# Performance work log

Hardware: AMD Instinct MI355X
Metric: run time of the kernel (lower is better)

Reference implementation:

```python
import jax, jax.numpy as jnp
import numpy as np

FILTER_K = 100  # filter_K from __init__
NUM_CLASSES = 1000


def setup_inputs() -> dict:
    key = jax.random.key(0)
    ks = jax.random.split(key, 7)
    B, Din, D, C, N = 256, 2048, 512, NUM_CLASSES, 50000
    x = jax.random.normal(ks[0], (B, Din), jnp.float32)
    Wf = jax.random.normal(ks[1], (Din, D), jnp.float32) * 0.02
    Wc = jax.random.normal(ks[2], (C, D), jnp.float32) * 0.05
    bc = jax.random.normal(ks[3], (C,), jnp.float32) * 0.01
    supports_in = jax.random.normal(ks[4], (N, D), jnp.float32)
    ent_in = jax.random.uniform(ks[5], (N,), jnp.float32)
    labels_idx = jax.random.randint(ks[6], (N,), 0, C)
    return {"x": x, "Wf": Wf, "Wc": Wc, "bc": bc,
            "supports_in": supports_in, "ent_in": ent_in, "labels_idx": labels_idx}


def _softmax_entropy(logits):
    # -(softmax * log_softmax).sum(1), computed stably in one pass
    logp = jax.nn.log_softmax(logits, axis=1)
    return -(jnp.exp(logp) * logp).sum(axis=1)


def reference(x, Wf, Wc, bc, supports_in, ent_in, labels_idx):
    C = Wc.shape[0]
    z = x @ Wf                    # featurizer: [B, D]
    p = z @ Wc.T + bc             # classifier logits: [B, C]
    yhat = jax.nn.one_hot(jnp.argmax(p, axis=1), C, dtype=z.dtype)
    ent_new = _softmax_entropy(p)
    labels_in = jax.nn.one_hot(labels_idx, C, dtype=z.dtype)

    # grow support memory
    supports = jnp.concatenate([supports_in, z], axis=0)   # [M, D]
    labels = jnp.concatenate([labels_in, yhat], axis=0)    # [M, C]
    ent = jnp.concatenate([ent_in, ent_new], axis=0)       # [M]

    # select_supports: per-class keep FILTER_K lowest-entropy entries.
    # Torch gathers a variable-size subset; equivalent fixed-shape form is a
    # boolean mask (non-selected rows contribute zero to the weights matmul).
    y = jnp.argmax(labels, axis=1)
    M = ent.shape[0]
    order = jnp.lexsort((ent, y))            # sort by class, then entropy
    y_sorted = y[order]
    # rank of each entry within its class segment
    rank = jnp.arange(M) - jnp.searchsorted(y_sorted, y_sorted, side='left')
    mask = jnp.zeros((M,), bool).at[order].set(rank < FILTER_K)
    maskf = mask.astype(z.dtype)

    # normalize supports row-wise (F.normalize, eps=1e-12), then masked matmul
    s_norm = supports / jnp.maximum(
        jnp.linalg.norm(supports, axis=1, keepdims=True), 1e-12)
    weights = (s_norm * maskf[:, None]).T @ (labels * maskf[:, None])  # [D, C]
    weights = weights / jnp.maximum(
        jnp.linalg.norm(weights, axis=0, keepdims=True), 1e-12)
    return z @ weights            # [B, C]
```

## Files before the change

kernel.cpp:

```cpp
#include <hip/hip_runtime.h>
#include <hip/hip_bf16.h>
#include <math.h>

#define BB   256
#define DIN  2048
#define DD   512
#define CC   1000
#define NN   50000
#define MM   (NN + BB)
#define FILTER_K 100
#define SLOT 512

#define SK1  32
#define SKP  8

#define Z_OFF     0
#define CNT_OFF   (Z_OFF + BB*DD)
#define ENTS_OFF  (CNT_OFF + 1024)
#define IDXS_OFF  (ENTS_OFF + CC*SLOT)
#define WN_OFF    (IDXS_OFF + CC*SLOT)
#define ZP_OFF    (WN_OFF + CC*DD)
#define PP_OFF    (ZP_OFF + SK1*BB*DD)

__global__ __launch_bounds__(256, 2) void fused_scatter_gemm_ab(
    const float* __restrict__ A, const float* __restrict__ B,
    float* __restrict__ Cp,
    const int* __restrict__ labels_idx, const float* __restrict__ ent_in,
    int* __restrict__ cnt, float* __restrict__ ent_s,
    int* __restrict__ idx_s) {
  __shared__ float As[16][68];
  __shared__ float Bs[16][132];
  const int gbid = blockIdx.x, tid = threadIdx.x;
  if (gbid >= 512) {
    int m = (gbid - 512) * 256 + tid;
    if (m < NN) {
      int c = labels_idx[m];
      int pos = atomicAdd(&cnt[c], 1);
      if (pos < SLOT) {
        ent_s[(size_t)c * SLOT + pos] = ent_in[m];
        idx_s[(size_t)c * SLOT + pos] = m;
      }
    }
    return;
  }
  const int m0 = ((gbid >> 2) & 3) * 64;
  const int n0 = (gbid & 3) * 128;
  const int k0 = (gbid >> 4) * 64;
  const int ar = tid >> 2, ac = (tid & 3) * 4;
  const int br = tid >> 4, bcn = (tid & 15) * 8;
  const int tm = (tid >> 4) * 4, tn = (tid & 15) * 4;
  float acc[4][8] = {};
  float4 av  = *(const float4*)&A[(size_t)(m0 + ar) * DIN + k0 + ac];
  float4 bv0 = *(const float4*)&B[(size_t)(k0 + br) * DD + n0 + bcn];
  float4 bv1 = *(const float4*)&B[(size_t)(k0 + br) * DD + n0 + bcn + 4];
  for (int kk = 0; kk < 64; kk += 16) {
    __syncthreads();
    As[ac + 0][ar] = av.x; As[ac + 1][ar] = av.y;
    As[ac + 2][ar] = av.z; As[ac + 3][ar] = av.w;
    *(float4*)&Bs[br][bcn] = bv0;
    *(float4*)&Bs[br][bcn + 4] = bv1;
    __syncthreads();
    if (kk + 16 < 64) {
      av  = *(const float4*)&A[(size_t)(m0 + ar) * DIN + k0 + kk + 16 + ac];
      bv0 = *(const float4*)&B[(size_t)(k0 + kk + 16 + br) * DD + n0 + bcn];
      bv1 = *(const float4*)&B[(size_t)(k0 + kk + 16 + br) * DD + n0 + bcn + 4];
    }
#pragma unroll
    for (int q = 0; q < 16; ++q) {
      float4 a  = *(const float4*)&As[q][tm];
      float4 b0 = *(const float4*)&Bs[q][tn];
      float4 b1 = *(const float4*)&Bs[q][tn + 64];
      float aa[4] = {a.x, a.y, a.z, a.w};
      float bb[8] = {b0.x, b0.y, b0.z, b0.w, b1.x, b1.y, b1.z, b1.w};
#pragma unroll
      for (int i = 0; i < 4; ++i)
#pragma unroll
        for (int j = 0; j < 8; ++j) acc[i][j] += aa[i] * bb[j];
    }
  }
  float* Cb = Cp + (size_t)(gbid >> 4) * BB * DD;
#pragma unroll
  for (int i = 0; i < 4; ++i) {
    *(float4*)&Cb[(size_t)(m0 + tm + i) * DD + n0 + tn] =
        make_float4(acc[i][0], acc[i][1], acc[i][2], acc[i][3]);
    *(float4*)&Cb[(size_t)(m0 + tm + i) * DD + n0 + 64 + tn] =
        make_float4(acc[i][4], acc[i][5], acc[i][6], acc[i][7]);
  }
}

template <int S>
__global__ __launch_bounds__(256) void reduce_part(
    const float* __restrict__ part, float* __restrict__ out, int n4) {
  int i = blockIdx.x * 256 + threadIdx.x;
  if (i >= n4) return;
  const float4* p4 = (const float4*)part;
  float4 a = p4[i];
#pragma unroll
  for (int s = 1; s < S; ++s) {
    float4 b = p4[(size_t)s * n4 + i];
    a.x += b.x; a.y += b.y; a.z += b.z; a.w += b.w;
  }
  ((float4*)out)[i] = a;
}

__global__ __launch_bounds__(256, 2) void gemm_abt_part(
    const float* __restrict__ A, const float* __restrict__ Bm,
    float* __restrict__ Cp) {
  __shared__ float As[16][68];
  __shared__ float Bs[16][68];
  const int tid = threadIdx.x;
  const int m0 = blockIdx.y * 64;
  const int n0 = blockIdx.x * 64;
  const int k0 = blockIdx.z * 64;
  const int ar = tid >> 2, ac = (tid & 3) * 4;
  const int tm = (tid >> 4) * 4, tn = (tid & 15) * 4;
  float acc[4][4] = {};
  float4 av = *(const float4*)&A[(size_t)(m0 + ar) * DD + k0 + ac];
  float4 bv = make_float4(0.f, 0.f, 0.f, 0.f);
  if (n0 + ar < CC) bv = *(const float4*)&Bm[(size_t)(n0 + ar) * DD + k0 + ac];
  for (int kk = 0; kk < 64; kk += 16) {
    __syncthreads();
    As[ac + 0][ar] = av.x; As[ac + 1][ar] = av.y;
    As[ac + 2][ar] = av.z; As[ac + 3][ar] = av.w;
    Bs[ac + 0][ar] = bv.x; Bs[ac + 1][ar] = bv.y;
    Bs[ac + 2][ar] = bv.z; Bs[ac + 3][ar] = bv.w;
    __syncthreads();
    if (kk + 16 < 64) {
      av = *(const float4*)&A[(size_t)(m0 + ar) * DD + k0 + kk + 16 + ac];
      if (n0 + ar < CC)
        bv = *(const float4*)&Bm[(size_t)(n0 + ar) * DD + k0 + kk + 16 + ac];
    }
#pragma unroll
    for (int q = 0; q < 16; ++q) {
      float4 a = *(const float4*)&As[q][tm];
      float4 b = *(const float4*)&Bs[q][tn];
      float aa[4] = {a.x, a.y, a.z, a.w};
      float bb[4] = {b.x, b.y, b.z, b.w};
#pragma unroll
      for (int i = 0; i < 4; ++i)
#pragma unroll
        for (int j = 0; j < 4; ++j) acc[i][j] += aa[i] * bb[j];
    }
  }
  float* Cb = Cp + (size_t)blockIdx.z * BB * CC;
#pragma unroll
  for (int i = 0; i < 4; ++i) {
    int n = n0 + tn;
    if (n + 3 < CC) {
      *(float4*)&Cb[(size_t)(m0 + tm + i) * CC + n] =
          make_float4(acc[i][0], acc[i][1], acc[i][2], acc[i][3]);
    } else {
#pragma unroll
      for (int j = 0; j < 4; ++j)
        if (n + j < CC) Cb[(size_t)(m0 + tm + i) * CC + n + j] = acc[i][j];
    }
  }
}

__global__ __launch_bounds__(256) void rowstats(
    const float* __restrict__ ppart, const float* __restrict__ bc,
    int* __restrict__ cnt, float* __restrict__ ent_s,
    int* __restrict__ idx_s) {
  const int b = blockIdx.x, tid = threadIdx.x;
  const int lane = tid & 63, wid = tid >> 6;
  float r[4];
  float mv = -INFINITY; int mi = 0x7fffffff;
#pragma unroll
  for (int i = 0; i < 4; ++i) {
    int c = tid + 256 * i;
    if (c < CC) {
      float v = bc[c];
#pragma unroll
      for (int s = 0; s < SKP; ++s)
        v += ppart[(size_t)s * BB * CC + (size_t)b * CC + c];
      r[i] = v;
    } else r[i] = -INFINITY;
    if (r[i] > mv) { mv = r[i]; mi = c; }
  }
#pragma unroll
  for (int o = 32; o > 0; o >>= 1) {
    float ov = __shfl_down(mv, o, 64);
    int oi = __shfl_down(mi, o, 64);
    if (ov > mv || (ov == mv && oi < mi)) { mv = ov; mi = oi; }
  }
  __shared__ float smv[4]; __shared__ int smi[4];
  __shared__ float ssm[4], tsm[4];
  if (lane == 0) { smv[wid] = mv; smi[wid] = mi; }
  __syncthreads();
  if (tid == 0) {
#pragma unroll
    for (int w = 1; w < 4; ++w)
      if (smv[w] > smv[0] || (smv[w] == smv[0] && smi[w] < smi[0])) {
        smv[0] = smv[w]; smi[0] = smi[w];
      }
  }
  __syncthreads();
  const float m = smv[0]; const int am = smi[0];
  float s = 0.f, t = 0.f;
#pragma unroll
  for (int i = 0; i < 4; ++i) {
    if (tid + 256 * i < CC) {
      float u = r[i] - m;
      float e = expf(u);
      s += e; t += u * e;
    }
  }
#pragma unroll
  for (int o = 32; o > 0; o >>= 1) {
    s += __shfl_down(s, o, 64);
    t += __shfl_down(t, o, 64);
  }
  if (lane == 0) { ssm[wid] = s; tsm[wid] = t; }
  __syncthreads();
  if (tid == 0) {
    float S = ssm[0] + ssm[1] + ssm[2] + ssm[3];
    float T = tsm[0] + tsm[1] + tsm[2] + tsm[3];
    float ent = logf(S) - T / S;
    int pos = atomicAdd(&cnt[am], 1);
    if (pos < SLOT) {
      ent_s[(size_t)am * SLOT + pos] = ent;
      idx_s[(size_t)am * SLOT + pos] = NN + b;
    }
  }
}

__global__ __launch_bounds__(256) void class_weights(
    const float* __restrict__ supports_in, const float* __restrict__ z,
    const float* __restrict__ ent_s, const int* __restrict__ idx_s,
    const int* __restrict__ cnt, float* __restrict__ wn) {
  const int c = blockIdx.x, tid = threadIdx.x;
  const int lane = tid & 63, wid = tid >> 6;
  int n = cnt[c]; if (n > SLOT) n = SLOT;

  __shared__ int sel[SLOT];
  __shared__ float se[SLOT];
  __shared__ int si[SLOT];
  int seln;
  if (n <= FILTER_K) {
    seln = n;
    for (int i = tid; i < n; i += 256) sel[i] = idx_s[(size_t)c * SLOT + i];
  } else {
    for (int i = tid; i < SLOT; i += 256) {
      if (i < n) { se[i] = ent_s[(size_t)c * SLOT + i]; si[i] = idx_s[(size_t)c * SLOT + i]; }
      else       { se[i] = INFINITY;                     si[i] = 0x7fffffff; }
    }
    __syncthreads();
    for (int k = 2; k <= SLOT; k <<= 1)
      for (int j = k >> 1; j > 0; j >>= 1) {
        for (int i = tid; i < SLOT; i += 256) {
          int ixj = i ^ j;
          if (ixj > i) {
            bool up = ((i & k) == 0);
            float e1 = se[i], e2 = se[ixj];
            int i1 = si[i], i2 = si[ixj];
            bool gt = (e1 > e2) || (e1 == e2 && i1 > i2);
            if (gt == up) { se[i] = e2; se[ixj] = e1; si[i] = i2; si[ixj] = i1; }
          }
        }
        __syncthreads();
      }
    seln = FILTER_K;
    for (int i = tid; i < FILTER_K; i += 256) sel[i] = si[i];
  }
  __syncthreads();
  const int seln_pad = (seln + 15) & ~15;
  if (seln > 0)
    for (int i = seln + tid; i < seln_pad; i += 256) sel[i] = sel[0];
  __syncthreads();

  float4 a0 = make_float4(0.f, 0.f, 0.f, 0.f), a1 = a0;
  for (int t = wid * 4; t < seln_pad; t += 16) {
    float4 u0[4], u1[4]; float s[4];
#pragma unroll
    for (int j = 0; j < 4; ++j) {
      int r = sel[t + j];
      const float4* p4 = (const float4*)((r < NN)
          ? supports_in + (size_t)r * DD : z + (size_t)(r - NN) * DD);
      u0[j] = p4[lane * 2]; u1[j] = p4[lane * 2 + 1];
    }
#pragma unroll
    for (int j = 0; j < 4; ++j)
      s[j] = u0[j].x * u0[j].x + u0[j].y * u0[j].y + u0[j].z * u0[j].z
           + u0[j].w * u0[j].w + u1[j].x * u1[j].x + u1[j].y * u1[j].y
           + u1[j].z * u1[j].z + u1[j].w * u1[j].w;
#pragma unroll
    for (int o = 1; o < 64; o <<= 1) {
#pragma unroll
      for (int j = 0; j < 4; ++j) s[j] += __shfl_xor(s[j], o, 64);
    }
#pragma unroll
    for (int j = 0; j < 4; ++j) {
      float sc = (t + j < seln) ? 1.0f / fmaxf(sqrtf(s[j]), 1e-12f) : 0.f;
      a0.x += u0[j].x * sc; a0.y += u0[j].y * sc;
      a0.z += u0[j].z * sc; a0.w += u0[j].w * sc;
      a1.x += u1[j].x * sc; a1.y += u1[j].y * sc;
      a1.z += u1[j].z * sc; a1.w += u1[j].w * sc;
    }
  }

  __shared__ float part[4][DD];
  *(float4*)&part[wid][lane * 8] = a0;
  *(float4*)&part[wid][lane * 8 + 4] = a1;
  __syncthreads();
  const int d = tid * 2;
  float wx = part[0][d] + part[1][d] + part[2][d] + part[3][d];
  float wy = part[0][d + 1] + part[1][d + 1] + part[2][d + 1] + part[3][d + 1];
  float ss = wx * wx + wy * wy;
#pragma unroll
  for (int o = 1; o < 64; o <<= 1) ss += __shfl_xor(ss, o, 64);
  __shared__ float tot[4];
  if (lane == 0) tot[wid] = ss;
  __syncthreads();
  float S = tot[0] + tot[1] + tot[2] + tot[3];
  float sc = 1.0f / fmaxf(sqrtf(S), 1e-12f);
  ((float2*)(wn + (size_t)c * DD))[tid] = make_float2(wx * sc, wy * sc);
}

__global__ __launch_bounds__(256, 2) void gemm_out(
    const float* __restrict__ A, const float* __restrict__ Bm,
    float* __restrict__ C) {
  __shared__ float As[16][36];
  __shared__ float Bs[16][68];
  const int tid = threadIdx.x;
  const int m0 = blockIdx.y * 32;
  const int n0 = blockIdx.x * 64;
  const int ar = tid >> 3, ac = (tid & 7) * 2;
  const int br = tid >> 2, bc = (tid & 3) * 4;
  const int tm = (tid >> 4) * 2, tn = (tid & 15) * 4;
  float acc[2][4] = {};
  float2 av = *(const float2*)&A[(size_t)(m0 + ar) * DD + ac];
  float4 bv = make_float4(0.f, 0.f, 0.f, 0.f);
  if (n0 + br < CC) bv = *(const float4*)&Bm[(size_t)(n0 + br) * DD + bc];
  for (int k0 = 0; k0 < DD; k0 += 16) {
    __syncthreads();
    As[ac + 0][ar] = av.x; As[ac + 1][ar] = av.y;
    Bs[bc + 0][br] = bv.x; Bs[bc + 1][br] = bv.y;
    Bs[bc + 2][br] = bv.z; Bs[bc + 3][br] = bv.w;
    __syncthreads();
    if (k0 + 16 < DD) {
      av = *(const float2*)&A[(size_t)(m0 + ar) * DD + k0 + 16 + ac];
      if (n0 + br < CC)
        bv = *(const float4*)&Bm[(size_t)(n0 + br) * DD + k0 + 16 + bc];
    }
#pragma unroll
    for (int q = 0; q < 16; ++q) {
      float2 a = *(const float2*)&As[q][tm];
      float4 b = *(const float4*)&Bs[q][tn];
      float aa[2] = {a.x, a.y};
      float bb[4] = {b.x, b.y, b.z, b.w};
#pragma unroll
      for (int i = 0; i < 2; ++i)
#pragma unroll
        for (int j = 0; j < 4; ++j) acc[i][j] += aa[i] * bb[j];
    }
  }
#pragma unroll
  for (int i = 0; i < 2; ++i) {
    int n = n0 + tn;
    if (n + 3 < CC) {
      *(float4*)&C[(size_t)(m0 + tm + i) * CC + n] =
          make_float4(acc[i][0], acc[i][1], acc[i][2], acc[i][3]);
    } else {
#pragma unroll
      for (int j = 0; j < 4; ++j)
        if (n + j < CC) C[(size_t)(m0 + tm + i) * CC + n + j] = acc[i][j];
    }
  }
}

extern "C" void kernel_launch(void* const* d_in, const int* in_sizes, int n_in,
                              void* d_out, int out_size, void* d_ws, size_t ws_size,
                              hipStream_t stream) {
  (void)in_sizes; (void)n_in; (void)out_size; (void)ws_size;
  const float* x           = (const float*)d_in[0];
  const float* Wf          = (const float*)d_in[1];
  const float* Wc          = (const float*)d_in[2];
  const float* bc          = (const float*)d_in[3];
  const float* supports_in = (const float*)d_in[4];
  const float* ent_in      = (const float*)d_in[5];
  const int*   labels_idx  = (const int*)d_in[6];
  float* out = (float*)d_out;

  float* W = (float*)d_ws;
  float* z     = W + Z_OFF;
  int*   cnt   = (int*)(W + CNT_OFF);
  float* ent_s = W + ENTS_OFF;
  int*   idx_s = (int*)(W + IDXS_OFF);
  float* wn    = W + WN_OFF;
  float* zpart = W + ZP_OFF;
  float* ppart = W + PP_OFF;

  hipMemsetAsync(cnt, 0, 1024 * sizeof(int), stream);
  fused_scatter_gemm_ab<<<512 + (NN + 255) / 256, 256, 0, stream>>>(
      x, Wf, zpart, labels_idx, ent_in, cnt, ent_s, idx_s);
  reduce_part<SK1><<<(BB * DD / 4 + 255) / 256, 256, 0, stream>>>(
      zpart, z, BB * DD / 4);
  gemm_abt_part<<<dim3((CC + 63) / 64, BB / 64, SKP), 256, 0, stream>>>(
      z, Wc, ppart);
  rowstats<<<BB, 256, 0, stream>>>(ppart, bc, cnt, ent_s, idx_s);
  class_weights<<<CC, 256, 0, stream>>>(supports_in, z, ent_s, idx_s, cnt, wn);
  gemm_out<<<dim3((CC + 63) / 64, BB / 32), 256, 0, stream>>>(z, wn, out);
}
```

Baseline: 228.3 us.

## Halve split-K partitions, pad atomic counters, pack entropy-index pairs as float2

Doubles the per-block K extent in both split-K GEMMs, halving the number of partial buffers and the reduction work in reduce_part and rowstats. Spreads per-class atomic counters across 16-int strides so that atomics on different classes do not contend on the same cache line. Stores each entropy/index pair as one float2 so that scatter and gather use one 8-byte access instead of two separate arrays. The cost is fewer blocks per GEMM, and therefore less parallelism, plus a larger counter memset.

```diff
diff --git a/kernel.cpp b/kernel.cpp
--- a/kernel.cpp
+++ b/kernel.cpp
@@ -10,15 +10,15 @@
 #define MM   (NN + BB)
 #define FILTER_K 100
 #define SLOT 512
-
-#define SK1  32
-#define SKP  8
+#define CSTRIDE 16
+
+#define SK1  16
+#define SKP  4
 
 #define Z_OFF     0
 #define CNT_OFF   (Z_OFF + BB*DD)
-#define ENTS_OFF  (CNT_OFF + 1024)
-#define IDXS_OFF  (ENTS_OFF + CC*SLOT)
-#define WN_OFF    (IDXS_OFF + CC*SLOT)
+#define EI_OFF    (CNT_OFF + 1024*CSTRIDE)
+#define WN_OFF    (EI_OFF + CC*SLOT*2)
 #define ZP_OFF    (WN_OFF + CC*DD)
 #define PP_OFF    (ZP_OFF + SK1*BB*DD)
 
@@ -26,26 +26,25 @@
     const float* __restrict__ A, const float* __restrict__ B,
     float* __restrict__ Cp,
     const int* __restrict__ labels_idx, const float* __restrict__ ent_in,
-    int* __restrict__ cnt, float* __restrict__ ent_s,
-    int* __restrict__ idx_s) {
+    int* __restrict__ cnt, float2* __restrict__ ei) {
   __shared__ float As[16][68];
   __shared__ float Bs[16][132];
   const int gbid = blockIdx.x, tid = threadIdx.x;
-  if (gbid >= 512) {
-    int m = (gbid - 512) * 256 + tid;
+  if (gbid >= 256) {
+    int m = (gbid - 256) * 256 + tid;
     if (m < NN) {
       int c = labels_idx[m];
-      int pos = atomicAdd(&cnt[c], 1);
+      int pos = atomicAdd(&cnt[c * CSTRIDE], 1);
       if (pos < SLOT) {
-        ent_s[(size_t)c * SLOT + pos] = ent_in[m];
-        idx_s[(size_t)c * SLOT + pos] = m;
+        float2 pr; pr.x = ent_in[m]; pr.y = __int_as_float(m);
+        ei[(size_t)c * SLOT + pos] = pr;
       }
     }
     return;
   }
   const int m0 = ((gbid >> 2) & 3) * 64;
   const int n0 = (gbid & 3) * 128;
-  const int k0 = (gbid >> 4) * 64;
+  const int k0 = (gbid >> 4) * 128;
   const int ar = tid >> 2, ac = (tid & 3) * 4;
   const int br = tid >> 4, bcn = (tid & 15) * 8;
   const int tm = (tid >> 4) * 4, tn = (tid & 15) * 4;
@@ -53,14 +52,14 @@
   float4 av  = *(const float4*)&A[(size_t)(m0 + ar) * DIN + k0 + ac];
   float4 bv0 = *(const float4*)&B[(size_t)(k0 + br) * DD + n0 + bcn];
   float4 bv1 = *(const float4*)&B[(size_t)(k0 + br) * DD + n0 + bcn + 4];
-  for (int kk = 0; kk < 64; kk += 16) {
+  for (int kk = 0; kk < 128; kk += 16) {
     __syncthreads();
     As[ac + 0][ar] = av.x; As[ac + 1][ar] = av.y;
     As[ac + 2][ar] = av.z; As[ac + 3][ar] = av.w;
     *(float4*)&Bs[br][bcn] = bv0;
     *(float4*)&Bs[br][bcn + 4] = bv1;
     __syncthreads();
-    if (kk + 16 < 64) {
+    if (kk + 16 < 128) {
       av  = *(const float4*)&A[(size_t)(m0 + ar) * DIN + k0 + kk + 16 + ac];
       bv0 = *(const float4*)&B[(size_t)(k0 + kk + 16 + br) * DD + n0 + bcn];
       bv1 = *(const float4*)&B[(size_t)(k0 + kk + 16 + br) * DD + n0 + bcn + 4];
@@ -111,21 +110,21 @@
   const int tid = threadIdx.x;
   const int m0 = blockIdx.y * 64;
   const int n0 = blockIdx.x * 64;
-  const int k0 = blockIdx.z * 64;
+  const int k0 = blockIdx.z * 128;
   const int ar = tid >> 2, ac = (tid & 3) * 4;
   const int tm = (tid >> 4) * 4, tn = (tid & 15) * 4;
   float acc[4][4] = {};
   float4 av = *(const float4*)&A[(size_t)(m0 + ar) * DD + k0 + ac];
   float4 bv = make_float4(0.f, 0.f, 0.f, 0.f);
   if (n0 + ar < CC) bv = *(const float4*)&Bm[(size_t)(n0 + ar) * DD + k0 + ac];
-  for (int kk = 0; kk < 64; kk += 16) {
+  for (int kk = 0; kk < 128; kk += 16) {
     __syncthreads();
     As[ac + 0][ar] = av.x; As[ac + 1][ar] = av.y;
     As[ac + 2][ar] = av.z; As[ac + 3][ar] = av.w;
     Bs[ac + 0][ar] = bv.x; Bs[ac + 1][ar] = bv.y;
     Bs[ac + 2][ar] = bv.z; Bs[ac + 3][ar] = bv.w;
     __syncthreads();
-    if (kk + 16 < 64) {
+    if (kk + 16 < 128) {
       av = *(const float4*)&A[(size_t)(m0 + ar) * DD + k0 + kk + 16 + ac];
       if (n0 + ar < CC)
         bv = *(const float4*)&Bm[(size_t)(n0 + ar) * DD + k0 + kk + 16 + ac];
@@ -159,8 +158,7 @@
 
 __global__ __launch_bounds__(256) void rowstats(
     const float* __restrict__ ppart, const float* __restrict__ bc,
-    int* __restrict__ cnt, float* __restrict__ ent_s,
-    int* __restrict__ idx_s) {
+    int* __restrict__ cnt, float2* __restrict__ ei) {
   const int b = blockIdx.x, tid = threadIdx.x;
   const int lane = tid & 63, wid = tid >> 6;
   float r[4];
@@ -216,21 +214,21 @@
     float S = ssm[0] + ssm[1] + ssm[2] + ssm[3];
     float T = tsm[0] + tsm[1] + tsm[2] + tsm[3];
     float ent = logf(S) - T / S;
-    int pos = atomicAdd(&cnt[am], 1);
+    int pos = atomicAdd(&cnt[am * CSTRIDE], 1);
     if (pos < SLOT) {
-      ent_s[(size_t)am * SLOT + pos] = ent;
-      idx_s[(size_t)am * SLOT + pos] = NN + b;
+      float2 pr; pr.x = ent; pr.y = __int_as_float(NN + b);
+      ei[(size_t)am * SLOT + pos] = pr;
     }
   }
 }
 
 __global__ __launch_bounds__(256) void class_weights(
     const float* __restrict__ supports_in, const float* __restrict__ z,
-    const float* __restrict__ ent_s, const int* __restrict__ idx_s,
-    const int* __restrict__ cnt, float* __restrict__ wn) {
+    const float2* __restrict__ ei, const int* __restrict__ cnt,
+    float* __restrict__ wn) {
   const int c = blockIdx.x, tid = threadIdx.x;
   const int lane = tid & 63, wid = tid >> 6;
-  int n = cnt[c]; if (n > SLOT) n = SLOT;
+  int n = cnt[c * CSTRIDE]; if (n > SLOT) n = SLOT;
 
   __shared__ int sel[SLOT];
   __shared__ float se[SLOT];
@@ -238,11 +236,14 @@
   int seln;
   if (n <= FILTER_K) {
     seln = n;
-    for (int i = tid; i < n; i += 256) sel[i] = idx_s[(size_t)c * SLOT + i];
+    for (int i = tid; i < n; i += 256)
+      sel[i] = __float_as_int(ei[(size_t)c * SLOT + i].y);
   } else {
     for (int i = tid; i < SLOT; i += 256) {
-      if (i < n) { se[i] = ent_s[(size_t)c * SLOT + i]; si[i] = idx_s[(size_t)c * SLOT + i]; }
-      else       { se[i] = INFINITY;                     si[i] = 0x7fffffff; }
+      if (i < n) {
+        float2 pr = ei[(size_t)c * SLOT + i];
+        se[i] = pr.x; si[i] = __float_as_int(pr.y);
+      } else { se[i] = INFINITY; si[i] = 0x7fffffff; }
     }
     __syncthreads();
     for (int k = 2; k <= SLOT; k <<= 1)
@@ -382,22 +383,21 @@
   float* out = (float*)d_out;
 
   float* W = (float*)d_ws;
-  float* z     = W + Z_OFF;
-  int*   cnt   = (int*)(W + CNT_OFF);
-  float* ent_s = W + ENTS_OFF;
-  int*   idx_s = (int*)(W + IDXS_OFF);
-  float* wn    = W + WN_OFF;
-  float* zpart = W + ZP_OFF;
-  float* ppart = W + PP_OFF;
-
-  hipMemsetAsync(cnt, 0, 1024 * sizeof(int), stream);
-  fused_scatter_gemm_ab<<<512 + (NN + 255) / 256, 256, 0, stream>>>(
-      x, Wf, zpart, labels_idx, ent_in, cnt, ent_s, idx_s);
+  float*  z     = W + Z_OFF;
+  int*    cnt   = (int*)(W + CNT_OFF);
+  float2* ei    = (float2*)(W + EI_OFF);
+  float*  wn    = W + WN_OFF;
+  float*  zpart = W + ZP_OFF;
+  float*  ppart = W + PP_OFF;
+
+  hipMemsetAsync(cnt, 0, 1024 * CSTRIDE * sizeof(int), stream);
+  fused_scatter_gemm_ab<<<256 + (NN + 255) / 256, 256, 0, stream>>>(
+      x, Wf, zpart, labels_idx, ent_in, cnt, ei);
   reduce_part<SK1><<<(BB * DD / 4 + 255) / 256, 256, 0, stream>>>(
       zpart, z, BB * DD / 4);
   gemm_abt_part<<<dim3((CC + 63) / 64, BB / 64, SKP), 256, 0, stream>>>(
       z, Wc, ppart);
-  rowstats<<<BB, 256, 0, stream>>>(ppart, bc, cnt, ent_s, idx_s);
-  class_weights<<<CC, 256, 0, stream>>>(supports_in, z, ent_s, idx_s, cnt, wn);
+  rowstats<<<BB, 256, 0, stream>>>(ppart, bc, cnt, ei);
+  class_weights<<<CC, 256, 0, stream>>>(supports_in, z, ei, cnt, wn);
   gemm_out<<<dim3((CC + 63) / 64, BB / 32), 256, 0, stream>>>(z, wn, out);
 }
```

After: 221.8 us. -2.9%, faster.
